# Kernel optimization log

Hardware: AMD Instinct MI355X
Metric: run time of the kernel (lower is better)

## Reference

```python
import jax, jax.numpy as jnp
import numpy as np

B, S, C, H, F = 4, 2048, 256, 8, 512  # scenes, pillars/scene, embed, heads, ffn hidden
D = C // H


def setup_inputs() -> dict:
    key = jax.random.key(0)
    ks = jax.random.split(key, 6)
    n = lambda k, sh: jax.random.normal(k, sh, jnp.float32) * 0.02
    # batch index sorted, equal-size contiguous segments per scene
    bidx = (jnp.arange(B * S, dtype=jnp.int32) // S)[:, None]
    coords = jnp.concatenate([bidx, jnp.zeros((B * S, 3), jnp.int32)], axis=1)
    return dict(
        pillar_features=jax.random.normal(ks[0], (B * S, C), jnp.float32),
        voxel_coords=coords,
        w_qkv=n(ks[1], (3 * C, C)), b_qkv=jnp.zeros((3 * C,), jnp.float32),
        w_out=n(ks[2], (C, C)), b_out=jnp.zeros((C,), jnp.float32),
        ln1_g=jnp.ones((C,), jnp.float32), ln1_b=jnp.zeros((C,), jnp.float32),
        w1=n(ks[3], (F, C)), b1=jnp.zeros((F,), jnp.float32),
        w2=n(ks[4], (C, F)), b2=jnp.zeros((C,), jnp.float32),
        ln2_g=jnp.ones((C,), jnp.float32), ln2_b=jnp.zeros((C,), jnp.float32),
    )


def _ln(x, g, b):
    m = x.mean(-1, keepdims=True)
    v = x.var(-1, keepdims=True)  # biased var, matches torch LayerNorm
    return (x - m) / jnp.sqrt(v + 1e-5) * g + b


def reference(pillar_features, voxel_coords, w_qkv, b_qkv, w_out, b_out,
              ln1_g, ln1_b, w1, b1, w2, b2, ln2_g, ln2_b):
    # coords[:,0] is sorted with equal-size contiguous segments, so the
    # per-batch mask-gather in the original is exactly a reshape here.
    x = pillar_features.reshape(B, S, C)
    qkv = x @ w_qkv.T + b_qkv                      # [B,S,3C]
    q, k, v = jnp.split(qkv, 3, axis=-1)
    rs = lambda t: t.reshape(B, S, H, D).transpose(0, 2, 1, 3)  # [B,H,S,D]
    q, k, v = rs(q), rs(k), rs(v)
    scores = jnp.einsum('bhqd,bhkd->bhqk', q, k) / jnp.sqrt(jnp.float32(D))
    att = jax.nn.softmax(scores, axis=-1)
    o = jnp.einsum('bhqk,bhkd->bhqd', att, v).transpose(0, 2, 1, 3).reshape(B, S, C)
    o = o @ w_out.T + b_out
    x = _ln(x + o, ln1_g, ln1_b)
    f = jax.nn.gelu(x @ w1.T + b1, approximate=False) @ w2.T + b2
    x = _ln(x + f, ln2_g, ln2_b)
    return x.reshape(B * S, C)
```

## Files before the change

### kernel.cpp

```cpp
#include <hip/hip_runtime.h>
#include <math.h>

#define MROWS 8192
#define BATCH 4
#define SEQ   2048
#define CDIM  256
#define HEADS 8
#define DHEAD 32
#define FDIM  512
#define QKVN  768

typedef __attribute__((ext_vector_type(8))) short bf16x8;
typedef __attribute__((ext_vector_type(4))) float f32x4;

__device__ __forceinline__ unsigned pk_bf16(float a, float b) {
  unsigned r;
  asm("v_cvt_pk_bf16_f32 %0, %1, %2" : "=v"(r) : "v"(a), "v"(b));
  return r;
}
__device__ __forceinline__ float bf2f(short s) {
  unsigned u = ((unsigned)(unsigned short)s) << 16;
  return __builtin_bit_cast(float, u);
}
__device__ __forceinline__ short f2bf(float f) {
  unsigned u = __builtin_bit_cast(unsigned, f);
  u = (u + 0x7FFFu + ((u >> 16) & 1u)) >> 16;
  return (short)u;
}
__device__ __forceinline__ float fexp2(float x) {
#if __has_builtin(__builtin_amdgcn_exp2f)
  return __builtin_amdgcn_exp2f(x);
#else
  return exp2f(x);
#endif
}
__device__ __forceinline__ void gl16(const void* g, void* l) {
  __builtin_amdgcn_global_load_lds(
      (const __attribute__((address_space(1))) void*)g,
      (__attribute__((address_space(3))) void*)l, 16, 0, 0);
}
__device__ __forceinline__ float gelu_tanh(float v) {
  const float u = v * (0.7978845608f + 0.0356774081f * v * v);
  const float t = fexp2(u * 2.885390082f);
  return v * t / (t + 1.0f);
}

__global__ __launch_bounds__(256) void cast_all_k(
    const float* __restrict__ pillar, short* __restrict__ pb,
    const float* __restrict__ wq, short* __restrict__ wqb,
    const float* __restrict__ wo, short* __restrict__ wob,
    const float* __restrict__ w1, short* __restrict__ w1b,
    const float* __restrict__ w2, short* __restrict__ w2b)
{
  const int i = blockIdx.x * 256 + threadIdx.x;
  const float* s; short* d; int off;
  if (i < 524288)      { s = pillar; d = pb;  off = i; }
  else if (i < 573440) { s = wq;     d = wqb; off = i - 524288; }
  else if (i < 589824) { s = wo;     d = wob; off = i - 573440; }
  else if (i < 622592) { s = w1;     d = w1b; off = i - 589824; }
  else                 { s = w2;     d = w2b; off = i - 622592; }
  float4 v = reinterpret_cast<const float4*>(s)[off];
  uint2 o = { pk_bf16(v.x, v.y), pk_bf16(v.z, v.w) };
  *reinterpret_cast<uint2*>(d + off*4) = o;
}

template<int K, bool BF16OUT, bool GELU, bool VOUT>
__global__ __launch_bounds__(256) void gemm64_k(
    const short* __restrict__ A, const short* __restrict__ W,
    const float* __restrict__ bias, void* __restrict__ out,
    short* __restrict__ vt, int NS)
{
  __shared__ short AS[2][4096];
  __shared__ short WS[2][4096];
  const int tid = threadIdx.x;
  const int l   = tid & 63;
  const int w   = tid >> 6;
  const int m0 = blockIdx.x * 64;
  const int n0 = blockIdx.y * 64;
  const int wr = (w >> 1) * 32;
  const int wc = (w & 1) * 32;
  const int lr = l & 15;
  const int lg = l >> 4;

  f32x4 acc[2][2];
#pragma unroll
  for (int i = 0; i < 2; ++i)
#pragma unroll
    for (int j = 0; j < 2; ++j) acc[i][j] = (f32x4){0.f,0.f,0.f,0.f};

  auto stage = [&](int buf, int k0) {
#pragma unroll
    for (int i = 0; i < 2; ++i) {
      const int c = i*256 + tid;
      const int r = c >> 3;
      const int s = (c & 7) ^ (r & 7);
      gl16(A + (size_t)(m0 + r)*K + k0 + s*8, &AS[buf][c*8]);
      gl16(W + (size_t)(n0 + r)*K + k0 + s*8, &WS[buf][c*8]);
    }
  };

  stage(0, 0);
  const int NST = K / 64;
  for (int t = 0; t < NST; ++t) {
    const int buf = t & 1;
    __syncthreads();
    if (t + 1 < NST) stage(buf ^ 1, (t+1)*64);
#pragma unroll
    for (int ks = 0; ks < 2; ++ks) {
      const int sl = ((ks*4 + lg) ^ (lr & 7)) << 3;
      bf16x8 a[2], b[2];
#pragma unroll
      for (int mi = 0; mi < 2; ++mi)
        a[mi] = *reinterpret_cast<const bf16x8*>(&AS[buf][(wr + mi*16 + lr)*64 + sl]);
#pragma unroll
      for (int nj = 0; nj < 2; ++nj)
        b[nj] = *reinterpret_cast<const bf16x8*>(&WS[buf][(wc + nj*16 + lr)*64 + sl]);
#pragma unroll
      for (int mi = 0; mi < 2; ++mi)
#pragma unroll
        for (int nj = 0; nj < 2; ++nj)
          acc[mi][nj] = __builtin_amdgcn_mfma_f32_16x16x32_bf16(b[nj], a[mi], acc[mi][nj], 0, 0, 0);
    }
  }

#pragma unroll
  for (int mi = 0; mi < 2; ++mi) {
    const size_t m = m0 + wr + mi*16 + lr;
#pragma unroll
    for (int nj = 0; nj < 2; ++nj) {
      const int nf = n0 + wc + nj*16 + lg*4;
      float4 bs = *reinterpret_cast<const float4*>(&bias[nf]);
      f32x4 v = acc[mi][nj];
      float v0 = v[0]+bs.x, v1 = v[1]+bs.y, v2 = v[2]+bs.z, v3 = v[3]+bs.w;
      if (GELU) { v0 = gelu_tanh(v0); v1 = gelu_tanh(v1); v2 = gelu_tanh(v2); v3 = gelu_tanh(v3); }
      if (VOUT && n0 >= 512) {
        const int nl = nf - 512;
        const int hh = nl >> 5, dvb = nl & 31;
        const int bb = (int)(m >> 11), ss = (int)(m & 2047);
        short* vp = vt + ((size_t)((bb*8 + hh)*32 + dvb))*2048 + ss;
        vp[0] = f2bf(v0); vp[2048] = f2bf(v1); vp[4096] = f2bf(v2); vp[6144] = f2bf(v3);
      } else if (BF16OUT) {
        uint2 p = { pk_bf16(v0, v1), pk_bf16(v2, v3) };
        *reinterpret_cast<uint2*>((short*)out + m*NS + nf) = p;
      } else {
        float4 p = { v0, v1, v2, v3 };
        *reinterpret_cast<float4*>((float*)out + m*NS + nf) = p;
      }
    }
  }
}

__global__ __launch_bounds__(256) void attn_mfma_k(
    const short* __restrict__ qk, const short* __restrict__ vtg,
    short* __restrict__ attno)
{
  __shared__ short KS[2][2048];
  __shared__ short VS[2][2048];

  const int tid  = threadIdx.x;
  const int lane = tid & 63;
  const int wv   = tid >> 6;
  const int bh   = blockIdx.x;
  const int b    = bh >> 3, h = bh & 7;
  const int q0   = blockIdx.y * 64 + wv * 16;

  const int lr = lane & 15;
  const int lg = lane >> 4;

  bf16x8 qf;
  {
    bf16x8 qraw = *reinterpret_cast<const bf16x8*>(
        qk + (size_t)(b*SEQ + q0 + lr)*512 + h*DHEAD + lg*8);
    const float c = 0.25508134f;
#pragma unroll
    for (int j = 0; j < 8; ++j) qf[j] = f2bf(bf2f(qraw[j]) * c);
  }

  f32x4 o0 = {0.f,0.f,0.f,0.f}, o1 = {0.f,0.f,0.f,0.f};
  float lsum = 0.f;

  const short* kSrc;
  {
    const int r = tid >> 2, s = tid & 3;
    const int rr = r & 31;
    const int key = ((rr >> 2) & 3)*8 + ((rr >> 4) & 1)*4 + (rr & 3) + (r & 32);
    const int slog = s ^ ((r >> 1) & 3);
    kSrc = qk + (size_t)(b*SEQ + key)*512 + 256 + h*DHEAD + slog*8;
  }
  const short* vSrc;
  {
    const int r = tid >> 3, s = tid & 7;
    const int slog = s ^ (r & 7);
    vSrc = vtg + ((size_t)(bh*32 + r))*2048 + slog*8;
  }

  gl16(kSrc, &KS[0][tid*8]);
  gl16(vSrc, &VS[0][tid*8]);
  kSrc += 64*512; vSrc += 64;

  const int kxor = (lr >> 1) & 3;
  const int vxor = lr & 7;

  for (int t = 0; t < SEQ/64; ++t) {
    const int buf = t & 1;
    __syncthreads();
    if (t + 1 < SEQ/64) {
      gl16(kSrc, &KS[buf^1][tid*8]);
      gl16(vSrc, &VS[buf^1][tid*8]);
      kSrc += 64*512; vSrc += 64;
    }

#pragma unroll
    for (int half = 0; half < 2; ++half) {
      const int krow = (half*32 + lr)*32 + ((lg ^ kxor) << 3);
      bf16x8 kf0 = *reinterpret_cast<const bf16x8*>(&KS[buf][krow]);
      bf16x8 kf1 = *reinterpret_cast<const bf16x8*>(&KS[buf][krow + 512]);
      f32x4 z = {0.f,0.f,0.f,0.f};
      f32x4 s0 = __builtin_amdgcn_mfma_f32_16x16x32_bf16(kf0, qf, z, 0, 0, 0);
      f32x4 s1 = __builtin_amdgcn_mfma_f32_16x16x32_bf16(kf1, qf, z, 0, 0, 0);

      const int vcol = (((half*4 + lg) ^ vxor) << 3);
      bf16x8 vf0 = *reinterpret_cast<const bf16x8*>(&VS[buf][lr*64 + vcol]);
      bf16x8 vf1 = *reinterpret_cast<const bf16x8*>(&VS[buf][(lr+16)*64 + vcol]);

      float p0 = fexp2(s0[0]), p1 = fexp2(s0[1]), p2 = fexp2(s0[2]), p3 = fexp2(s0[3]);
      float p4 = fexp2(s1[0]), p5 = fexp2(s1[1]), p6 = fexp2(s1[2]), p7 = fexp2(s1[3]);
      lsum += ((p0+p1)+(p2+p3)) + ((p4+p5)+(p6+p7));
      union { bf16x8 v; unsigned w[4]; } pfu;
      pfu.w[0] = pk_bf16(p0, p1); pfu.w[1] = pk_bf16(p2, p3);
      pfu.w[2] = pk_bf16(p4, p5); pfu.w[3] = pk_bf16(p6, p7);

      o0 = __builtin_amdgcn_mfma_f32_16x16x32_bf16(vf0, pfu.v, o0, 0, 0, 0);
      o1 = __builtin_amdgcn_mfma_f32_16x16x32_bf16(vf1, pfu.v, o1, 0, 0, 0);
    }
  }

  lsum += __shfl_xor(lsum, 16);
  lsum += __shfl_xor(lsum, 32);
  const float inv = 1.f / lsum;

  short* op = attno + (size_t)(b*SEQ + q0 + lr)*CDIM + h*DHEAD;
  uint2 r0 = { pk_bf16(o0[0]*inv, o0[1]*inv), pk_bf16(o0[2]*inv, o0[3]*inv) };
  uint2 r1 = { pk_bf16(o1[0]*inv, o1[1]*inv), pk_bf16(o1[2]*inv, o1[3]*inv) };
  *reinterpret_cast<uint2*>(op + lg*4)      = r0;
  *reinterpret_cast<uint2*>(op + 16 + lg*4) = r1;
}

template<bool WB>
__global__ __launch_bounds__(256) void resid_ln_k(
    const float* __restrict__ x, const float* __restrict__ y,
    const float* __restrict__ g, const float* __restrict__ bta,
    float* __restrict__ out, short* __restrict__ outb)
{
  const int row  = blockIdx.x * 4 + (threadIdx.x >> 6);
  const int lane = threadIdx.x & 63;
  const int c0   = lane * 4;
  const size_t base = (size_t)row * CDIM + c0;
  float4 xv = *reinterpret_cast<const float4*>(&x[base]);
  float4 yv = *reinterpret_cast<const float4*>(&y[base]);
  float4 v = { xv.x+yv.x, xv.y+yv.y, xv.z+yv.z, xv.w+yv.w };
  float s  = v.x + v.y + v.z + v.w;
  float sq = v.x*v.x + v.y*v.y + v.z*v.z + v.w*v.w;
#pragma unroll
  for (int off = 1; off < 64; off <<= 1) {
    s  += __shfl_xor(s,  off);
    sq += __shfl_xor(sq, off);
  }
  const float mean = s * (1.f/CDIM);
  const float var  = sq * (1.f/CDIM) - mean*mean;
  const float rstd = rsqrtf(var + 1e-5f);
  float4 gv = *reinterpret_cast<const float4*>(&g[c0]);
  float4 bv = *reinterpret_cast<const float4*>(&bta[c0]);
  float4 r = { (v.x-mean)*rstd*gv.x + bv.x, (v.y-mean)*rstd*gv.y + bv.y,
               (v.z-mean)*rstd*gv.z + bv.z, (v.w-mean)*rstd*gv.w + bv.w };
  *reinterpret_cast<float4*>(&out[base]) = r;
  if (WB) {
    uint2 p = { pk_bf16(r.x, r.y), pk_bf16(r.z, r.w) };
    *reinterpret_cast<uint2*>(outb + base) = p;
  }
}

extern "C" void kernel_launch(void* const* d_in, const int* in_sizes, int n_in,
                              void* d_out, int out_size, void* d_ws, size_t ws_size,
                              hipStream_t stream)
{
  const float* pillar = (const float*)d_in[0];
  const float* w_qkv  = (const float*)d_in[2];
  const float* b_qkv  = (const float*)d_in[3];
  const float* w_out  = (const float*)d_in[4];
  const float* b_out  = (const float*)d_in[5];
  const float* ln1_g  = (const float*)d_in[6];
  const float* ln1_b  = (const float*)d_in[7];
  const float* w1     = (const float*)d_in[8];
  const float* b1     = (const float*)d_in[9];
  const float* w2     = (const float*)d_in[10];
  const float* b2     = (const float*)d_in[11];
  const float* ln2_g  = (const float*)d_in[12];
  const float* ln2_b  = (const float*)d_in[13];
  float* out = (float*)d_out;
  short* sb  = (short*)d_ws;

  short* pb    = sb;
  short* wqb   = sb + 2097152;
  short* wob   = sb + 2293760;
  short* w1b   = sb + 2359296;
  short* w2b   = sb + 2490368;
  short* qk    = sb + 2621440;
  short* vtg   = sb + 6815744;
  short* attnb = sb + 8912896;
  short* x1b   = sb + 2621440;
  short* yhidb = sb + 4718592;
  float* fp    = (float*)(sb + 11010048);
  float* ptmp  = fp;
  float* x1    = fp + 2097152;
  float* f2    = ptmp;

  cast_all_k<<<2560, 256, 0, stream>>>(pillar, pb, w_qkv, wqb, w_out, wob,
                                       w1, w1b, w2, w2b);

  gemm64_k<CDIM, true, false, true><<<dim3(MROWS/64, QKVN/64), 256, 0, stream>>>(
      pb, wqb, b_qkv, qk, vtg, 512);

  attn_mfma_k<<<dim3(BATCH*HEADS, SEQ/64), 256, 0, stream>>>(qk, vtg, attnb);

  gemm64_k<CDIM, false, false, false><<<dim3(MROWS/64, CDIM/64), 256, 0, stream>>>(
      attnb, wob, b_out, ptmp, nullptr, CDIM);

  resid_ln_k<true><<<dim3(MROWS/4), 256, 0, stream>>>(pillar, ptmp, ln1_g, ln1_b, x1, x1b);

  gemm64_k<CDIM, true, true, false><<<dim3(MROWS/64, FDIM/64), 256, 0, stream>>>(
      x1b, w1b, b1, yhidb, nullptr, FDIM);

  gemm64_k<FDIM, false, false, false><<<dim3(MROWS/64, CDIM/64), 256, 0, stream>>>(
      yhidb, w2b, b2, f2, nullptr, CDIM);

  resid_ln_k<false><<<dim3(MROWS/4), 256, 0, stream>>>(x1, f2, ln2_g, ln2_b, out, nullptr);
}
```

Measured before the change: 90.04 us.

## Split attention key range across two wave groups and compute row sums via MFMA

The attention kernel now launches 512 threads per block. Two groups of four waves each process half of the key sequence, and their partial outputs and softmax denominators are merged through shared memory at the end. The per-lane scalar row-sum accumulation is replaced by an extra MFMA against a vector of ones, which removes the final cross-lane shuffles. This shortens each wave's serial loop and doubles the number of resident waves, at the cost of twice the LDS per block, one extra MFMA per step and a merge phase.

```diff
diff --git a/kernel.cpp b/kernel.cpp
--- a/kernel.cpp
+++ b/kernel.cpp
@@ -150,19 +150,21 @@
   }
 }
 
-__global__ __launch_bounds__(256) void attn_mfma_k(
+__global__ __launch_bounds__(512, 8) void attn_mfma_k(
     const short* __restrict__ qk, const short* __restrict__ vtg,
     short* __restrict__ attno)
 {
-  __shared__ short KS[2][2048];
-  __shared__ short VS[2][2048];
+  __shared__ short KS[2][2][2048];
+  __shared__ short VS[2][2][2048];
 
   const int tid  = threadIdx.x;
   const int lane = tid & 63;
   const int wv   = tid >> 6;
+  const int st   = wv >> 2;
+  const int qw   = wv & 3;
   const int bh   = blockIdx.x;
   const int b    = bh >> 3, h = bh & 7;
-  const int q0   = blockIdx.y * 64 + wv * 16;
+  const int q0   = blockIdx.y * 64 + qw * 16;
 
   const int lr = lane & 15;
   const int lg = lane >> 4;
@@ -175,75 +177,91 @@
 #pragma unroll
     for (int j = 0; j < 8; ++j) qf[j] = f2bf(bf2f(qraw[j]) * c);
   }
+  bf16x8 ones;
+#pragma unroll
+  for (int j = 0; j < 8; ++j) ones[j] = (short)0x3F80;
 
   f32x4 o0 = {0.f,0.f,0.f,0.f}, o1 = {0.f,0.f,0.f,0.f};
-  float lsum = 0.f;
-
+  f32x4 lacc = {0.f,0.f,0.f,0.f};
+
+  const int t256 = tid & 255;
   const short* kSrc;
   {
-    const int r = tid >> 2, s = tid & 3;
+    const int r = t256 >> 2, s = t256 & 3;
     const int rr = r & 31;
     const int key = ((rr >> 2) & 3)*8 + ((rr >> 4) & 1)*4 + (rr & 3) + (r & 32);
     const int slog = s ^ ((r >> 1) & 3);
-    kSrc = qk + (size_t)(b*SEQ + key)*512 + 256 + h*DHEAD + slog*8;
+    kSrc = qk + (size_t)(b*SEQ + st*1024 + key)*512 + 256 + h*DHEAD + slog*8;
   }
   const short* vSrc;
   {
-    const int r = tid >> 3, s = tid & 7;
+    const int r = t256 >> 3, s = t256 & 7;
     const int slog = s ^ (r & 7);
-    vSrc = vtg + ((size_t)(bh*32 + r))*2048 + slog*8;
-  }
-
-  gl16(kSrc, &KS[0][tid*8]);
-  gl16(vSrc, &VS[0][tid*8]);
+    vSrc = vtg + ((size_t)(bh*32 + r))*2048 + st*1024 + slog*8;
+  }
+
+  gl16(kSrc, &KS[st][0][t256*8]);
+  gl16(vSrc, &VS[st][0][t256*8]);
   kSrc += 64*512; vSrc += 64;
 
   const int kxor = (lr >> 1) & 3;
   const int vxor = lr & 7;
 
-  for (int t = 0; t < SEQ/64; ++t) {
+  for (int t = 0; t < 16; ++t) {
     const int buf = t & 1;
     __syncthreads();
-    if (t + 1 < SEQ/64) {
-      gl16(kSrc, &KS[buf^1][tid*8]);
-      gl16(vSrc, &VS[buf^1][tid*8]);
+    if (t + 1 < 16) {
+      gl16(kSrc, &KS[st][buf^1][t256*8]);
+      gl16(vSrc, &VS[st][buf^1][t256*8]);
       kSrc += 64*512; vSrc += 64;
     }
 
 #pragma unroll
     for (int half = 0; half < 2; ++half) {
       const int krow = (half*32 + lr)*32 + ((lg ^ kxor) << 3);
-      bf16x8 kf0 = *reinterpret_cast<const bf16x8*>(&KS[buf][krow]);
-      bf16x8 kf1 = *reinterpret_cast<const bf16x8*>(&KS[buf][krow + 512]);
+      bf16x8 kf0 = *reinterpret_cast<const bf16x8*>(&KS[st][buf][krow]);
+      bf16x8 kf1 = *reinterpret_cast<const bf16x8*>(&KS[st][buf][krow + 512]);
       f32x4 z = {0.f,0.f,0.f,0.f};
       f32x4 s0 = __builtin_amdgcn_mfma_f32_16x16x32_bf16(kf0, qf, z, 0, 0, 0);
       f32x4 s1 = __builtin_amdgcn_mfma_f32_16x16x32_bf16(kf1, qf, z, 0, 0, 0);
 
       const int vcol = (((half*4 + lg) ^ vxor) << 3);
-      bf16x8 vf0 = *reinterpret_cast<const bf16x8*>(&VS[buf][lr*64 + vcol]);
-      bf16x8 vf1 = *reinterpret_cast<const bf16x8*>(&VS[buf][(lr+16)*64 + vcol]);
+      bf16x8 vf0 = *reinterpret_cast<const bf16x8*>(&VS[st][buf][lr*64 + vcol]);
+      bf16x8 vf1 = *reinterpret_cast<const bf16x8*>(&VS[st][buf][(lr+16)*64 + vcol]);
 
       float p0 = fexp2(s0[0]), p1 = fexp2(s0[1]), p2 = fexp2(s0[2]), p3 = fexp2(s0[3]);
       float p4 = fexp2(s1[0]), p5 = fexp2(s1[1]), p6 = fexp2(s1[2]), p7 = fexp2(s1[3]);
-      lsum += ((p0+p1)+(p2+p3)) + ((p4+p5)+(p6+p7));
       union { bf16x8 v; unsigned w[4]; } pfu;
       pfu.w[0] = pk_bf16(p0, p1); pfu.w[1] = pk_bf16(p2, p3);
       pfu.w[2] = pk_bf16(p4, p5); pfu.w[3] = pk_bf16(p6, p7);
 
-      o0 = __builtin_amdgcn_mfma_f32_16x16x32_bf16(vf0, pfu.v, o0, 0, 0, 0);
-      o1 = __builtin_amdgcn_mfma_f32_16x16x32_bf16(vf1, pfu.v, o1, 0, 0, 0);
-    }
-  }
-
-  lsum += __shfl_xor(lsum, 16);
-  lsum += __shfl_xor(lsum, 32);
-  const float inv = 1.f / lsum;
-
-  short* op = attno + (size_t)(b*SEQ + q0 + lr)*CDIM + h*DHEAD;
-  uint2 r0 = { pk_bf16(o0[0]*inv, o0[1]*inv), pk_bf16(o0[2]*inv, o0[3]*inv) };
-  uint2 r1 = { pk_bf16(o1[0]*inv, o1[1]*inv), pk_bf16(o1[2]*inv, o1[3]*inv) };
-  *reinterpret_cast<uint2*>(op + lg*4)      = r0;
-  *reinterpret_cast<uint2*>(op + 16 + lg*4) = r1;
+      o0   = __builtin_amdgcn_mfma_f32_16x16x32_bf16(vf0, pfu.v, o0, 0, 0, 0);
+      o1   = __builtin_amdgcn_mfma_f32_16x16x32_bf16(vf1, pfu.v, o1, 0, 0, 0);
+      lacc = __builtin_amdgcn_mfma_f32_16x16x32_bf16(ones, pfu.v, lacc, 0, 0, 0);
+    }
+  }
+
+  __syncthreads();
+  float* mg = (float*)&KS[0][0][0];
+  const int mi = (qw*64 + lane)*10;
+  if (st == 1) {
+    mg[mi+0]=o0[0]; mg[mi+1]=o0[1]; mg[mi+2]=o0[2]; mg[mi+3]=o0[3];
+    mg[mi+4]=o1[0]; mg[mi+5]=o1[1]; mg[mi+6]=o1[2]; mg[mi+7]=o1[3];
+    mg[mi+8]=lacc[0];
+  }
+  __syncthreads();
+  if (st == 0) {
+    const float inv = 1.f / (lacc[0] + mg[mi+8]);
+    float a0 = (o0[0]+mg[mi+0])*inv, a1 = (o0[1]+mg[mi+1])*inv;
+    float a2 = (o0[2]+mg[mi+2])*inv, a3 = (o0[3]+mg[mi+3])*inv;
+    float b0 = (o1[0]+mg[mi+4])*inv, b1 = (o1[1]+mg[mi+5])*inv;
+    float b2 = (o1[2]+mg[mi+6])*inv, b3 = (o1[3]+mg[mi+7])*inv;
+    short* op = attno + (size_t)(b*SEQ + q0 + lr)*CDIM + h*DHEAD;
+    uint2 r0 = { pk_bf16(a0, a1), pk_bf16(a2, a3) };
+    uint2 r1 = { pk_bf16(b0, b1), pk_bf16(b2, b3) };
+    *reinterpret_cast<uint2*>(op + lg*4)      = r0;
+    *reinterpret_cast<uint2*>(op + 16 + lg*4) = r1;
+  }
 }
 
 template<bool WB>
@@ -321,7 +339,7 @@
   gemm64_k<CDIM, true, false, true><<<dim3(MROWS/64, QKVN/64), 256, 0, stream>>>(
       pb, wqb, b_qkv, qk, vtg, 512);
 
-  attn_mfma_k<<<dim3(BATCH*HEADS, SEQ/64), 256, 0, stream>>>(qk, vtg, attnb);
+  attn_mfma_k<<<dim3(BATCH*HEADS, SEQ/64), 512, 0, stream>>>(qk, vtg, attnb);
 
   gemm64_k<CDIM, false, false, false><<<dim3(MROWS/64, CDIM/64), 256, 0, stream>>>(
       attnb, wob, b_out, ptmp, nullptr, CDIM);
```

Result: faster. 83.08 us (-7.7%).
